# Optimization experiments

Measured on AMD Instinct MI355X. Metric: run time of the kernel, lower is better.

The kernel has to match this reference:

```python
import jax, jax.numpy as jnp
import numpy as np

GRID = 32  # hard-coded voxel resolution in the original module


def setup_inputs() -> dict:
    key = jax.random.key(0)
    k1, k2 = jax.random.split(key)
    points = jax.random.normal(k1, (4, 100000, 3), dtype=jnp.float32)
    features = jax.random.normal(k2, (4, 100000, 64), dtype=jnp.float32)
    return {"points": points, "features": features}


def reference(points, features):
    # points: [B, N, 3], features: [B, N, F]
    B, N, _ = points.shape
    Fdim = features.shape[-1]
    # Global (over whole tensor) min/max normalization, exactly as original
    pmin = points.min()
    pmax = points.max()
    normed = (points - pmin) / (pmax - pmin + 1e-6)  # in [0, 1)
    # torch: (normed // (1/32)).long() == floor(normed * 32)
    vox = jnp.floor(normed * GRID).astype(jnp.int32)  # [B, N, 3], values in [0, 31]
    gidx = vox[..., 0] * (GRID * GRID) + vox[..., 1] * GRID + vox[..., 2]  # [B, N]
    # Scatter-max into a zero-initialized grid (zeros init == implicit max with 0,
    # matching the original torch.zeros output_grid).
    grid = jnp.zeros((B, GRID ** 3, Fdim), dtype=features.dtype)
    batch_ids = jnp.arange(B, dtype=jnp.int32)[:, None]  # [B, 1] broadcast over N
    grid = grid.at[batch_ids, gidx].max(features)
    return grid.reshape(B, GRID, GRID, GRID, Fdim)
```

## Files before the change

kernel.cpp:

```cpp
#include <hip/hip_runtime.h>

#define GRID3 32768
#define FDIM 64
#define CHUNK 512

__device__ __forceinline__ unsigned int enc_f32(float f) {
    unsigned int u = __float_as_uint(f);
    return (u & 0x80000000u) ? ~u : (u | 0x80000000u);
}
__device__ __forceinline__ float dec_f32(unsigned int u) {
    u = (u & 0x80000000u) ? (u ^ 0x80000000u) : ~u;
    return __uint_as_float(u);
}

__device__ __forceinline__ int bin_of(float x, float y, float z,
                                      float pmin, float denom) {
    int vx = (int)(((x - pmin) / denom) * 32.0f);
    int vy = (int)(((y - pmin) / denom) * 32.0f);
    int vz = (int)(((z - pmin) / denom) * 32.0f);
    vx = min(max(vx, 0), 31);
    vy = min(max(vy, 0), 31);
    vz = min(max(vz, 0), 31);
    return (vx << 10) + (vy << 5) + vz;
}

__global__ void init_ws_kernel(unsigned int* ws) {
    ws[0] = 0xFFFFFFFFu;
    ws[1] = 0u;
}

__global__ void minmax_kernel(const float* __restrict__ pts, int n,
                              unsigned int* __restrict__ ws) {
    float lmin = INFINITY, lmax = -INFINITY;
    const float4* p4 = reinterpret_cast<const float4*>(pts);
    const int n4 = n >> 2;
    for (int i = blockIdx.x * blockDim.x + threadIdx.x; i < n4;
         i += gridDim.x * blockDim.x) {
        float4 v = p4[i];
        lmin = fminf(lmin, fminf(fminf(v.x, v.y), fminf(v.z, v.w)));
        lmax = fmaxf(lmax, fmaxf(fmaxf(v.x, v.y), fmaxf(v.z, v.w)));
    }
    for (int i = (n4 << 2) + blockIdx.x * blockDim.x + threadIdx.x; i < n;
         i += gridDim.x * blockDim.x) {
        float v = pts[i];
        lmin = fminf(lmin, v);
        lmax = fmaxf(lmax, v);
    }
    __shared__ float smin[256], smax[256];
    smin[threadIdx.x] = lmin;
    smax[threadIdx.x] = lmax;
    __syncthreads();
    for (int s = 128; s > 0; s >>= 1) {
        if (threadIdx.x < (unsigned)s) {
            smin[threadIdx.x] = fminf(smin[threadIdx.x], smin[threadIdx.x + s]);
            smax[threadIdx.x] = fmaxf(smax[threadIdx.x], smax[threadIdx.x + s]);
        }
        __syncthreads();
    }
    if (threadIdx.x == 0) {
        atomicMin(&ws[0], enc_f32(smin[0]));
        atomicMax(&ws[1], enc_f32(smax[0]));
    }
}

__global__ void count_kernel(const float* __restrict__ pts,
                             const unsigned int* __restrict__ ws,
                             unsigned int* __restrict__ cnt,
                             int ntot, int N) {
    int i = blockIdx.x * blockDim.x + threadIdx.x;
    if (i >= ntot) return;
    float pmin = dec_f32(ws[0]);
    float denom = dec_f32(ws[1]) - pmin + 1e-6f;
    int bin = (i / N) * GRID3 +
              bin_of(pts[i * 3], pts[i * 3 + 1], pts[i * 3 + 2], pmin, denom);
    atomicAdd(&cnt[bin], 1u);
}

__global__ __launch_bounds__(256)
void scanA_kernel(const unsigned int* __restrict__ cnt,
                  unsigned int* __restrict__ bsum, int nbins) {
    __shared__ unsigned int s[256];
    int base = blockIdx.x * CHUNK;
    int t = threadIdx.x;
    unsigned int a = (base + t < nbins) ? cnt[base + t] : 0u;
    unsigned int b = (base + t + 256 < nbins) ? cnt[base + t + 256] : 0u;
    s[t] = a + b;
    __syncthreads();
    for (int st = 128; st > 0; st >>= 1) {
        if (t < st) s[t] += s[t + st];
        __syncthreads();
    }
    if (t == 0) bsum[blockIdx.x] = s[0];
}

__global__ __launch_bounds__(1024)
void scanB_kernel(unsigned int* __restrict__ bsum, int nchunks) {
    __shared__ unsigned int s[1024];
    int t = threadIdx.x;
    unsigned int own = (t < nchunks) ? bsum[t] : 0u;
    s[t] = own;
    __syncthreads();
    for (int off = 1; off < 1024; off <<= 1) {
        unsigned int v = (t >= off) ? s[t - off] : 0u;
        __syncthreads();
        s[t] += v;
        __syncthreads();
    }
    if (t < nchunks) bsum[t] = s[t] - own;
}

__global__ __launch_bounds__(256)
void scanC_kernel(unsigned int* __restrict__ cnt,
                  const unsigned int* __restrict__ bsum, int nbins) {
    __shared__ unsigned int s[256];
    int t = threadIdx.x;
    int base = blockIdx.x * CHUNK;
    int i0 = base + 2 * t;
    unsigned int a = (i0 < nbins) ? cnt[i0] : 0u;
    unsigned int b = (i0 + 1 < nbins) ? cnt[i0 + 1] : 0u;
    unsigned int p = a + b;
    s[t] = p;
    __syncthreads();
    for (int off = 1; off < 256; off <<= 1) {
        unsigned int v = (t >= off) ? s[t - off] : 0u;
        __syncthreads();
        s[t] += v;
        __syncthreads();
    }
    unsigned int excl = s[t] - p + bsum[blockIdx.x];
    if (i0 < nbins) cnt[i0] = excl;
    if (i0 + 1 < nbins) cnt[i0 + 1] = excl + a;
}

__global__ void fill_kernel(const float* __restrict__ pts,
                            const unsigned int* __restrict__ ws,
                            unsigned int* __restrict__ cursor,
                            unsigned int* __restrict__ idx,
                            int ntot, int N) {
    int i = blockIdx.x * blockDim.x + threadIdx.x;
    if (i >= ntot) return;
    float pmin = dec_f32(ws[0]);
    float denom = dec_f32(ws[1]) - pmin + 1e-6f;
    int bin = (i / N) * GRID3 +
              bin_of(pts[i * 3], pts[i * 3 + 1], pts[i * 3 + 2], pmin, denom);
    unsigned int pos = atomicAdd(&cursor[bin], 1u);
    idx[pos] = (unsigned int)i;
}

__global__ __launch_bounds__(256)
void gather_kernel(const float* __restrict__ feat,
                   const unsigned int* __restrict__ cursor,
                   const unsigned int* __restrict__ idx,
                   float* __restrict__ out, int nbins) {
    int bin = blockIdx.x * 4 + (threadIdx.x >> 6);
    int lane = threadIdx.x & 63;
    if (bin >= nbins) return;

    unsigned int s = bin ? cursor[bin - 1] : 0u;
    unsigned int e = cursor[bin];
    const float* fl = feat + lane;
    float acc = 0.0f;
    unsigned int k = s;

    for (; k + 16 <= e; k += 16) {
        unsigned int p[16];
#pragma unroll
        for (int j = 0; j < 16; ++j) p[j] = idx[k + j];
        float f[16];
#pragma unroll
        for (int j = 0; j < 16; ++j) f[j] = fl[(size_t)p[j] * FDIM];
        float m = f[0];
#pragma unroll
        for (int j = 1; j < 16; ++j) m = fmaxf(m, f[j]);
        acc = fmaxf(acc, m);
    }
    for (; k + 4 <= e; k += 4) {
        unsigned int p0 = idx[k], p1 = idx[k + 1];
        unsigned int p2 = idx[k + 2], p3 = idx[k + 3];
        float f0 = fl[(size_t)p0 * FDIM];
        float f1 = fl[(size_t)p1 * FDIM];
        float f2 = fl[(size_t)p2 * FDIM];
        float f3 = fl[(size_t)p3 * FDIM];
        acc = fmaxf(acc, fmaxf(fmaxf(f0, f1), fmaxf(f2, f3)));
    }
    for (; k < e; ++k)
        acc = fmaxf(acc, fl[(size_t)idx[k] * FDIM]);
    out[(size_t)bin * FDIM + lane] = acc;
}

__global__ void scatter_kernel(const float* __restrict__ pts,
                               const float* __restrict__ feat,
                               const unsigned int* __restrict__ ws,
                               unsigned int* __restrict__ out,
                               int ntot, int N) {
    int lane = threadIdx.x & 63;
    int p = blockIdx.x * 4 + (threadIdx.x >> 6);
    if (p >= ntot) return;
    float pmin = dec_f32(ws[0]);
    float denom = dec_f32(ws[1]) - pmin + 1e-6f;
    int gidx = bin_of(pts[p * 3], pts[p * 3 + 1], pts[p * 3 + 2], pmin, denom);
    int b = p / N;
    float f = feat[(size_t)p * FDIM + lane];
    if (f > 0.0f) {
        unsigned int* addr = out + ((size_t)b * GRID3 + gidx) * FDIM + lane;
        atomicMax(addr, __float_as_uint(f));
    }
}

extern "C" void kernel_launch(void* const* d_in, const int* in_sizes, int n_in,
                              void* d_out, int out_size, void* d_ws, size_t ws_size,
                              hipStream_t stream) {
    const float* pts = (const float*)d_in[0];
    const float* feat = (const float*)d_in[1];
    unsigned int* ws = (unsigned int*)d_ws;

    int npts3 = in_sizes[0];
    int ntot = npts3 / 3;
    int B = out_size / (GRID3 * FDIM);
    int N = ntot / B;
    int nbins = B * GRID3;
    int nchunks = (nbins + CHUNK - 1) / CHUNK;

    unsigned int* bsum = ws + 64;
    unsigned int* cursor = bsum + 1024;
    unsigned int* idx = cursor + nbins;
    size_t need = (size_t)(64 + 1024 + nbins + ntot) * 4;

    hipLaunchKernelGGL(init_ws_kernel, dim3(1), dim3(1), 0, stream, ws);
    hipLaunchKernelGGL(minmax_kernel, dim3(512), dim3(256), 0, stream,
                       pts, npts3, ws);

    int pblocks = (ntot + 255) / 256;
    if (ws_size >= need && nchunks <= 1024) {
        hipMemsetAsync(cursor, 0, (size_t)nbins * 4, stream);
        hipLaunchKernelGGL(count_kernel, dim3(pblocks), dim3(256), 0, stream,
                           pts, ws, cursor, ntot, N);
        hipLaunchKernelGGL(scanA_kernel, dim3(nchunks), dim3(256), 0, stream,
                           cursor, bsum, nbins);
        hipLaunchKernelGGL(scanB_kernel, dim3(1), dim3(1024), 0, stream,
                           bsum, nchunks);
        hipLaunchKernelGGL(scanC_kernel, dim3(nchunks), dim3(256), 0, stream,
                           cursor, bsum, nbins);
        hipLaunchKernelGGL(fill_kernel, dim3(pblocks), dim3(256), 0, stream,
                           pts, ws, cursor, idx, ntot, N);
        hipLaunchKernelGGL(gather_kernel, dim3((nbins + 3) / 4), dim3(256), 0,
                           stream, feat, cursor, idx, (float*)d_out, nbins);
    } else {
        hipMemsetAsync(d_out, 0, (size_t)out_size * sizeof(float), stream);
        hipLaunchKernelGGL(scatter_kernel, dim3((ntot + 3) / 4), dim3(256), 0,
                           stream, pts, feat, ws, (unsigned int*)d_out, ntot, N);
    }
}
```

Measured before the change: 290.5 us.

## Gather only occupied voxels via compacted bin list after zero-filling output

```diff
diff --git a/kernel.cpp b/kernel.cpp
--- a/kernel.cpp
+++ b/kernel.cpp
@@ -3,6 +3,7 @@
 #define GRID3 32768
 #define FDIM 64
 #define CHUNK 512
+#define GBLOCKS 2048
 
 __device__ __forceinline__ unsigned int enc_f32(float f) {
     unsigned int u = __float_as_uint(f);
@@ -27,6 +28,7 @@
 __global__ void init_ws_kernel(unsigned int* ws) {
     ws[0] = 0xFFFFFFFFu;
     ws[1] = 0u;
+    ws[2] = 0u;
 }
 
 __global__ void minmax_kernel(const float* __restrict__ pts, int n,
@@ -74,6 +76,17 @@
     int bin = (i / N) * GRID3 +
               bin_of(pts[i * 3], pts[i * 3 + 1], pts[i * 3 + 2], pmin, denom);
     atomicAdd(&cnt[bin], 1u);
+}
+
+__global__ void compact_kernel(const unsigned int* __restrict__ cnt,
+                               unsigned int* __restrict__ occ,
+                               unsigned int* __restrict__ noccp, int nbins) {
+    int i = blockIdx.x * blockDim.x + threadIdx.x;
+    if (i >= nbins) return;
+    if (cnt[i] != 0u) {
+        unsigned int pos = atomicAdd(noccp, 1u);
+        occ[pos] = (unsigned int)i;
+    }
 }
 
 __global__ __launch_bounds__(256)
@@ -148,6 +161,43 @@
 }
 
 __global__ __launch_bounds__(256)
+void gatherocc_kernel(const float* __restrict__ feat,
+                      const unsigned int* __restrict__ cursor,
+                      const unsigned int* __restrict__ idx,
+                      const unsigned int* __restrict__ occ,
+                      const unsigned int* __restrict__ noccp,
+                      float* __restrict__ out) {
+    int wid = blockIdx.x * 4 + (threadIdx.x >> 6);
+    int lane = threadIdx.x & 63;
+    int nocc = (int)*noccp;
+    const int nwaves = GBLOCKS * 4;
+    const float* fl = feat + lane;
+
+    for (int w = wid; w < nocc; w += nwaves) {
+        int bin = (int)occ[w];
+        unsigned int s = bin ? cursor[bin - 1] : 0u;
+        unsigned int e = cursor[bin];
+        float acc = 0.0f;
+        unsigned int k = s;
+        for (; k + 16 <= e; k += 16) {
+            unsigned int p[16];
+#pragma unroll
+            for (int j = 0; j < 16; ++j) p[j] = idx[k + j];
+            float f[16];
+#pragma unroll
+            for (int j = 0; j < 16; ++j) f[j] = fl[(size_t)p[j] * FDIM];
+            float m = f[0];
+#pragma unroll
+            for (int j = 1; j < 16; ++j) m = fmaxf(m, f[j]);
+            acc = fmaxf(acc, m);
+        }
+        for (; k < e; ++k)
+            acc = fmaxf(acc, fl[(size_t)idx[k] * FDIM]);
+        out[(size_t)bin * FDIM + lane] = acc;
+    }
+}
+
+__global__ __launch_bounds__(256)
 void gather_kernel(const float* __restrict__ feat,
                    const unsigned int* __restrict__ cursor,
                    const unsigned int* __restrict__ idx,
@@ -155,13 +205,11 @@
     int bin = blockIdx.x * 4 + (threadIdx.x >> 6);
     int lane = threadIdx.x & 63;
     if (bin >= nbins) return;
-
     unsigned int s = bin ? cursor[bin - 1] : 0u;
     unsigned int e = cursor[bin];
     const float* fl = feat + lane;
     float acc = 0.0f;
     unsigned int k = s;
-
     for (; k + 16 <= e; k += 16) {
         unsigned int p[16];
 #pragma unroll
@@ -173,15 +221,6 @@
 #pragma unroll
         for (int j = 1; j < 16; ++j) m = fmaxf(m, f[j]);
         acc = fmaxf(acc, m);
-    }
-    for (; k + 4 <= e; k += 4) {
-        unsigned int p0 = idx[k], p1 = idx[k + 1];
-        unsigned int p2 = idx[k + 2], p3 = idx[k + 3];
-        float f0 = fl[(size_t)p0 * FDIM];
-        float f1 = fl[(size_t)p1 * FDIM];
-        float f2 = fl[(size_t)p2 * FDIM];
-        float f3 = fl[(size_t)p3 * FDIM];
-        acc = fmaxf(acc, fmaxf(fmaxf(f0, f1), fmaxf(f2, f3)));
     }
     for (; k < e; ++k)
         acc = fmaxf(acc, fl[(size_t)idx[k] * FDIM]);
@@ -224,14 +263,34 @@
     unsigned int* bsum = ws + 64;
     unsigned int* cursor = bsum + 1024;
     unsigned int* idx = cursor + nbins;
-    size_t need = (size_t)(64 + 1024 + nbins + ntot) * 4;
+    unsigned int* occ = idx + ntot;
+    size_t need_occ = (size_t)(64 + 1024 + 2 * (size_t)nbins + ntot) * 4;
+    size_t need_csr = (size_t)(64 + 1024 + nbins + (size_t)ntot) * 4;
 
     hipLaunchKernelGGL(init_ws_kernel, dim3(1), dim3(1), 0, stream, ws);
     hipLaunchKernelGGL(minmax_kernel, dim3(512), dim3(256), 0, stream,
                        pts, npts3, ws);
 
     int pblocks = (ntot + 255) / 256;
-    if (ws_size >= need && nchunks <= 1024) {
+    if (ws_size >= need_occ && nchunks <= 1024) {
+        hipMemsetAsync(cursor, 0, (size_t)nbins * 4, stream);
+        hipLaunchKernelGGL(count_kernel, dim3(pblocks), dim3(256), 0, stream,
+                           pts, ws, cursor, ntot, N);
+        hipLaunchKernelGGL(compact_kernel, dim3((nbins + 255) / 256), dim3(256),
+                           0, stream, cursor, occ, &ws[2], nbins);
+        hipLaunchKernelGGL(scanA_kernel, dim3(nchunks), dim3(256), 0, stream,
+                           cursor, bsum, nbins);
+        hipLaunchKernelGGL(scanB_kernel, dim3(1), dim3(1024), 0, stream,
+                           bsum, nchunks);
+        hipLaunchKernelGGL(scanC_kernel, dim3(nchunks), dim3(256), 0, stream,
+                           cursor, bsum, nbins);
+        hipLaunchKernelGGL(fill_kernel, dim3(pblocks), dim3(256), 0, stream,
+                           pts, ws, cursor, idx, ntot, N);
+        hipMemsetAsync(d_out, 0, (size_t)out_size * sizeof(float), stream);
+        hipLaunchKernelGGL(gatherocc_kernel, dim3(GBLOCKS), dim3(256), 0,
+                           stream, feat, cursor, idx, occ, &ws[2],
+                           (float*)d_out);
+    } else if (ws_size >= need_csr && nchunks <= 1024) {
         hipMemsetAsync(cursor, 0, (size_t)nbins * 4, stream);
         hipLaunchKernelGGL(count_kernel, dim3(pblocks), dim3(256), 0, stream,
                            pts, ws, cursor, ntot, N);
```

After: 292.0 us. No clear change (+0.5%).

## Gather only occupied voxels with float4 work items and cached bin ids

Applied to the files above, without the earlier changes.

```diff
diff --git a/kernel.cpp b/kernel.cpp
--- a/kernel.cpp
+++ b/kernel.cpp
@@ -3,6 +3,7 @@
 #define GRID3 32768
 #define FDIM 64
 #define CHUNK 512
+#define SPLIT 128u
 
 __device__ __forceinline__ unsigned int enc_f32(float f) {
     unsigned int u = __float_as_uint(f);
@@ -27,6 +28,7 @@
 __global__ void init_ws_kernel(unsigned int* ws) {
     ws[0] = 0xFFFFFFFFu;
     ws[1] = 0u;
+    ws[2] = 0u;
 }
 
 __global__ void minmax_kernel(const float* __restrict__ pts, int n,
@@ -66,13 +68,15 @@
 __global__ void count_kernel(const float* __restrict__ pts,
                              const unsigned int* __restrict__ ws,
                              unsigned int* __restrict__ cnt,
+                             unsigned int* __restrict__ pbin,
                              int ntot, int N) {
     int i = blockIdx.x * blockDim.x + threadIdx.x;
     if (i >= ntot) return;
     float pmin = dec_f32(ws[0]);
     float denom = dec_f32(ws[1]) - pmin + 1e-6f;
-    int bin = (i / N) * GRID3 +
-              bin_of(pts[i * 3], pts[i * 3 + 1], pts[i * 3 + 2], pmin, denom);
+    unsigned int bin = (unsigned int)((i / N) * GRID3 +
+        bin_of(pts[i * 3], pts[i * 3 + 1], pts[i * 3 + 2], pmin, denom));
+    pbin[i] = bin;
     atomicAdd(&cnt[bin], 1u);
 }
 
@@ -111,7 +115,9 @@
 
 __global__ __launch_bounds__(256)
 void scanC_kernel(unsigned int* __restrict__ cnt,
-                  const unsigned int* __restrict__ bsum, int nbins) {
+                  const unsigned int* __restrict__ bsum,
+                  uint4* __restrict__ occ4,
+                  unsigned int* __restrict__ noccp, int nbins) {
     __shared__ unsigned int s[256];
     int t = threadIdx.x;
     int base = blockIdx.x * CHUNK;
@@ -130,13 +136,89 @@
     unsigned int excl = s[t] - p + bsum[blockIdx.x];
     if (i0 < nbins) cnt[i0] = excl;
     if (i0 + 1 < nbins) cnt[i0 + 1] = excl + a;
-}
-
-__global__ void fill_kernel(const float* __restrict__ pts,
-                            const unsigned int* __restrict__ ws,
+
+    if (i0 < nbins && a) {
+        if (a <= SPLIT) {
+            unsigned int pos = atomicAdd(noccp, 1u);
+            occ4[pos] = make_uint4((unsigned int)i0, excl, excl + a, 0u);
+        } else {
+            for (unsigned int off = 0; off < a; off += SPLIT) {
+                unsigned int pos = atomicAdd(noccp, 1u);
+                occ4[pos] = make_uint4((unsigned int)i0, excl + off,
+                                       excl + min(off + SPLIT, a), 1u);
+            }
+        }
+    }
+    if (i0 + 1 < nbins && b) {
+        unsigned int st = excl + a;
+        if (b <= SPLIT) {
+            unsigned int pos = atomicAdd(noccp, 1u);
+            occ4[pos] = make_uint4((unsigned int)(i0 + 1), st, st + b, 0u);
+        } else {
+            for (unsigned int off = 0; off < b; off += SPLIT) {
+                unsigned int pos = atomicAdd(noccp, 1u);
+                occ4[pos] = make_uint4((unsigned int)(i0 + 1), st + off,
+                                       st + min(off + SPLIT, b), 1u);
+            }
+        }
+    }
+}
+
+__global__ void fill_kernel(const unsigned int* __restrict__ pbin,
                             unsigned int* __restrict__ cursor,
-                            unsigned int* __restrict__ idx,
-                            int ntot, int N) {
+                            unsigned int* __restrict__ idx, int ntot) {
+    int i = blockIdx.x * blockDim.x + threadIdx.x;
+    if (i >= ntot) return;
+    unsigned int bin = pbin[i];
+    unsigned int pos = atomicAdd(&cursor[bin], 1u);
+    idx[pos] = (unsigned int)i;
+}
+
+__global__ __launch_bounds__(256)
+void gatherg16_kernel(const float4* __restrict__ feat4,
+                      const uint4* __restrict__ occ4,
+                      const unsigned int* __restrict__ noccp,
+                      const unsigned int* __restrict__ idx,
+                      float4* __restrict__ out4) {
+    unsigned int gslot = blockIdx.x * 16u + (threadIdx.x >> 4);
+    int l16 = threadIdx.x & 15;
+    int gbase = threadIdx.x & 48;
+    unsigned int nocc = *noccp;
+    if (gslot >= nocc) return;
+
+    uint4 o = occ4[gslot];
+    unsigned int bin = o.x, s = o.y, e = o.z;
+
+    float4 acc = make_float4(0.f, 0.f, 0.f, 0.f);
+    for (unsigned int k = s; k < e; k += 16u) {
+        unsigned int pj = idx[min(k + (unsigned int)l16, e - 1u)];
+#pragma unroll
+        for (int j = 0; j < 16; ++j) {
+            unsigned int pt = __shfl(pj, gbase + j);
+            float4 f = feat4[(size_t)pt * 16 + l16];
+            acc.x = fmaxf(acc.x, f.x);
+            acc.y = fmaxf(acc.y, f.y);
+            acc.z = fmaxf(acc.z, f.z);
+            acc.w = fmaxf(acc.w, f.w);
+        }
+    }
+    if (o.w == 0u) {
+        out4[(size_t)bin * 16 + l16] = acc;
+    } else {
+        unsigned int* ob =
+            (unsigned int*)(out4 + (size_t)bin * 16 + l16);
+        if (acc.x > 0.f) atomicMax(ob + 0, __float_as_uint(acc.x));
+        if (acc.y > 0.f) atomicMax(ob + 1, __float_as_uint(acc.y));
+        if (acc.z > 0.f) atomicMax(ob + 2, __float_as_uint(acc.z));
+        if (acc.w > 0.f) atomicMax(ob + 3, __float_as_uint(acc.w));
+    }
+}
+
+__global__ void fillpts_kernel(const float* __restrict__ pts,
+                               const unsigned int* __restrict__ ws,
+                               unsigned int* __restrict__ cursor,
+                               unsigned int* __restrict__ idx,
+                               int ntot, int N) {
     int i = blockIdx.x * blockDim.x + threadIdx.x;
     if (i >= ntot) return;
     float pmin = dec_f32(ws[0]);
@@ -155,13 +237,11 @@
     int bin = blockIdx.x * 4 + (threadIdx.x >> 6);
     int lane = threadIdx.x & 63;
     if (bin >= nbins) return;
-
     unsigned int s = bin ? cursor[bin - 1] : 0u;
     unsigned int e = cursor[bin];
     const float* fl = feat + lane;
     float acc = 0.0f;
     unsigned int k = s;
-
     for (; k + 16 <= e; k += 16) {
         unsigned int p[16];
 #pragma unroll
@@ -174,18 +254,32 @@
         for (int j = 1; j < 16; ++j) m = fmaxf(m, f[j]);
         acc = fmaxf(acc, m);
     }
-    for (; k + 4 <= e; k += 4) {
-        unsigned int p0 = idx[k], p1 = idx[k + 1];
-        unsigned int p2 = idx[k + 2], p3 = idx[k + 3];
-        float f0 = fl[(size_t)p0 * FDIM];
-        float f1 = fl[(size_t)p1 * FDIM];
-        float f2 = fl[(size_t)p2 * FDIM];
-        float f3 = fl[(size_t)p3 * FDIM];
-        acc = fmaxf(acc, fmaxf(fmaxf(f0, f1), fmaxf(f2, f3)));
-    }
     for (; k < e; ++k)
         acc = fmaxf(acc, fl[(size_t)idx[k] * FDIM]);
     out[(size_t)bin * FDIM + lane] = acc;
+}
+
+__global__ __launch_bounds__(256)
+void scanCp_kernel(unsigned int* __restrict__ cnt,
+                   const unsigned int* __restrict__ bsum, int nbins) {
+    __shared__ unsigned int s[256];
+    int t = threadIdx.x;
+    int base = blockIdx.x * CHUNK;
+    int i0 = base + 2 * t;
+    unsigned int a = (i0 < nbins) ? cnt[i0] : 0u;
+    unsigned int b = (i0 + 1 < nbins) ? cnt[i0 + 1] : 0u;
+    unsigned int p = a + b;
+    s[t] = p;
+    __syncthreads();
+    for (int off = 1; off < 256; off <<= 1) {
+        unsigned int v = (t >= off) ? s[t - off] : 0u;
+        __syncthreads();
+        s[t] += v;
+        __syncthreads();
+    }
+    unsigned int excl = s[t] - p + bsum[blockIdx.x];
+    if (i0 < nbins) cnt[i0] = excl;
+    if (i0 + 1 < nbins) cnt[i0 + 1] = excl + a;
 }
 
 __global__ void scatter_kernel(const float* __restrict__ pts,
@@ -221,27 +315,58 @@
     int nbins = B * GRID3;
     int nchunks = (nbins + CHUNK - 1) / CHUNK;
 
+    int wi_cap = nbins + ntot / (int)SPLIT + 16;
+
     unsigned int* bsum = ws + 64;
     unsigned int* cursor = bsum + 1024;
     unsigned int* idx = cursor + nbins;
-    size_t need = (size_t)(64 + 1024 + nbins + ntot) * 4;
+    unsigned int* pbin = idx + ntot;
+    size_t occ_off = ((size_t)(64 + 1024 + nbins + 2 * (size_t)ntot) + 3) &
+                     ~(size_t)3;
+    uint4* occ4 = (uint4*)(ws + occ_off);
+    size_t need_g16 = (occ_off + 4 * (size_t)wi_cap) * 4;
+    size_t need_csr = (size_t)(64 + 1024 + nbins + (size_t)ntot) * 4;
 
     hipLaunchKernelGGL(init_ws_kernel, dim3(1), dim3(1), 0, stream, ws);
     hipLaunchKernelGGL(minmax_kernel, dim3(512), dim3(256), 0, stream,
                        pts, npts3, ws);
 
     int pblocks = (ntot + 255) / 256;
-    if (ws_size >= need && nchunks <= 1024) {
+    if (ws_size >= need_g16 && nchunks <= 1024) {
         hipMemsetAsync(cursor, 0, (size_t)nbins * 4, stream);
         hipLaunchKernelGGL(count_kernel, dim3(pblocks), dim3(256), 0, stream,
-                           pts, ws, cursor, ntot, N);
+                           pts, ws, cursor, pbin, ntot, N);
         hipLaunchKernelGGL(scanA_kernel, dim3(nchunks), dim3(256), 0, stream,
                            cursor, bsum, nbins);
         hipLaunchKernelGGL(scanB_kernel, dim3(1), dim3(1024), 0, stream,
                            bsum, nchunks);
         hipLaunchKernelGGL(scanC_kernel, dim3(nchunks), dim3(256), 0, stream,
+                           cursor, bsum, occ4, &ws[2], nbins);
+        hipLaunchKernelGGL(fill_kernel, dim3(pblocks), dim3(256), 0, stream,
+                           pbin, cursor, idx, ntot);
+        hipMemsetAsync(d_out, 0, (size_t)out_size * sizeof(float), stream);
+        int gblocks = (wi_cap + 15) / 16;
+        hipLaunchKernelGGL(gatherg16_kernel, dim3(gblocks), dim3(256), 0,
+                           stream, (const float4*)feat, occ4, &ws[2], idx,
+                           (float4*)d_out);
+    } else if (ws_size >= need_csr && nchunks <= 1024) {
+        hipMemsetAsync(cursor, 0, (size_t)nbins * 4, stream);
+        hipLaunchKernelGGL(count_kernel, dim3(pblocks), dim3(256), 0, stream,
+                           pts, ws, cursor, cursor , ntot, N);
+        hipMemsetAsync(cursor, 0, (size_t)nbins * 4, stream);
+        hipLaunchKernelGGL(scatter_kernel, dim3(1), dim3(64), 0, stream,
+                           pts, feat, ws, (unsigned int*)d_out, 0, N);
+        hipMemsetAsync(cursor, 0, (size_t)nbins * 4, stream);
+        hipLaunchKernelGGL(count_kernel, dim3(pblocks), dim3(256), 0, stream,
+                           pts, ws, cursor, idx ,
+                           ntot, N);
+        hipLaunchKernelGGL(scanA_kernel, dim3(nchunks), dim3(256), 0, stream,
                            cursor, bsum, nbins);
-        hipLaunchKernelGGL(fill_kernel, dim3(pblocks), dim3(256), 0, stream,
+        hipLaunchKernelGGL(scanB_kernel, dim3(1), dim3(1024), 0, stream,
+                           bsum, nchunks);
+        hipLaunchKernelGGL(scanCp_kernel, dim3(nchunks), dim3(256), 0, stream,
+                           cursor, bsum, nbins);
+        hipLaunchKernelGGL(fillpts_kernel, dim3(pblocks), dim3(256), 0, stream,
                            pts, ws, cursor, idx, ntot, N);
         hipLaunchKernelGGL(gather_kernel, dim3((nbins + 3) / 4), dim3(256), 0,
                            stream, feat, cursor, idx, (float*)d_out, nbins);
```

Measured after the change: 275.4 us. -5.2%, faster.
